# Kernel optimization log

Measured on AMD Instinct MI355X. Metric: run time of the kernel, lower is better.

Reference implementation:

```python
import jax, jax.numpy as jnp
import numpy as np

KS = 5
STRIDE = 1


def extract_patches(x, ks, s):
    # TF tf.image.extract_patches ordering: (row, col, channel) flattened
    B, H, W, C = x.shape
    oh = (H - ks) // s + 1
    ow = (W - ks) // s + 1
    cols = [x[:, i:i + (oh - 1) * s + 1:s, j:j + (ow - 1) * s + 1:s, :]
            for i in range(ks) for j in range(ks)]
    p = jnp.stack(cols, axis=3)  # [B, oh, ow, ks*ks, C]
    return p.reshape(B, oh * ow, ks * ks * C)


def setup_inputs() -> dict:
    key = jax.random.key(0)
    k1, k2, k3 = jax.random.split(key, 3)
    B, H, W, C, K = 32, 14, 14, 32, 64
    mu_in = jax.random.normal(k1, (B, H, W, C), dtype=jnp.float32)
    Sigma_in = jax.random.uniform(k2, (B, H * W, H * W, C), dtype=jnp.float32)
    w_mu = 0.05 * jax.random.normal(k3, (KS, KS, C, K), dtype=jnp.float32)
    w_sigma = jnp.full((K,), -2.2, dtype=jnp.float32)
    return {"mu_in": mu_in, "Sigma_in": Sigma_in, "w_mu": w_mu, "w_sigma": w_sigma}


def reference(mu_in, Sigma_in, w_mu, w_sigma):
    B, H, W, C = mu_in.shape
    ks = w_mu.shape[0]
    K = w_mu.shape[-1]
    s = STRIDE

    # mean path: standard conv2d, NHWC / HWIO
    mu_out = jax.lax.conv_general_dilated(
        mu_in, w_mu, (s, s), 'VALID',
        dimension_numbers=('NHWC', 'HWIO', 'NHWC'))

    # diag of Sigma_in over the two N dims: [B,N,N,C] -> [B,C,N] -> [B,H,W,C]
    diag_sigma = jnp.diagonal(Sigma_in, axis1=1, axis2=2)           # [B,C,N]
    diag_sigma = jnp.transpose(diag_sigma, (0, 2, 1)).reshape(B, H, W, C)

    dsg = extract_patches(diag_sigma, ks, s)                        # [B,P,M]
    P = dsg.shape[1]

    mu_cov_sq = (w_mu * w_mu).reshape(-1, K)                        # [M,K]
    v1 = dsg @ mu_cov_sq                                            # [B,P,K]

    sp = jnp.log1p(jnp.exp(w_sigma))                                # softplus, [K]
    tr = jnp.sum(dsg, axis=2, keepdims=True)                        # [B,P,1]
    diag_vals = v1 + sp[None, None, :] * tr                         # [B,P,K] (trace1 + mu_wT_sigmags_mu_w diags)

    mu_p = extract_patches(mu_in, ks, s)                            # [B,P,M]
    G = jnp.einsum('bpm,bqm->bpq', mu_p, mu_p)                      # [B,P,P]

    Sigma_out = sp[None, None, None, :] * G[..., None]              # [B,P,P,K]
    ip = jnp.arange(P)
    Sigma_out = Sigma_out.at[:, ip, ip, :].add(diag_vals)

    Sigma_out = jnp.where(jnp.isnan(Sigma_out), 0.0, Sigma_out)
    Sigma_out = jnp.where(jnp.isinf(Sigma_out), 0.0, Sigma_out)

    # TF set_diag acts on the LAST two dims ([P,K] inner matrices) -- reproduce exactly
    m = min(P, K)
    ii = jnp.arange(m)
    Sigma_out = Sigma_out.at[:, :, ii, ii].set(jnp.abs(Sigma_out[:, :, ii, ii]))
    return mu_out, Sigma_out
```

## Files before the change

### kernel.cpp

```cpp
#include <hip/hip_runtime.h>
#include <cmath>

typedef __attribute__((ext_vector_type(8))) short short8;
typedef __attribute__((ext_vector_type(4))) float f32x4;

#define NB 32
#define MU_OUT_SZ (NB*100*64)
#define LDAP 56

__device__ inline unsigned short f2bf(float f) {
  unsigned u = __builtin_bit_cast(unsigned, f);
  u += 0x7fffu + ((u >> 16) & 1u);
  return (unsigned short)(u >> 16);
}

__global__ __launch_bounds__(256) void prepW(
    const float* __restrict__ w_mu, const float* __restrict__ w_sigma,
    unsigned short* __restrict__ wf) {
  __shared__ float wsh[2048];
  const int ij = blockIdx.x, t = threadIdx.x;
  const float4* src = (const float4*)(w_mu + (size_t)ij * 2048);
  ((float4*)wsh)[t]       = src[t];
  ((float4*)wsh)[t + 256] = src[t + 256];
  __syncthreads();
#pragma unroll
  for (int id0 = 0; id0 < 512; id0 += 256) {
    const int id = id0 + t;
    const int kind = id >> 8;
    const int rest = id & 255;
    const int n = rest >> 6, l = rest & 63;
    const int col = n * 16 + (l & 15);
    const int m0 = (l >> 4) * 8;
    const float sp = log1pf(expf(w_sigma[col]));
    unsigned short v[8];
#pragma unroll
    for (int i = 0; i < 8; ++i) {
      const float wv = wsh[(m0 + i) * 64 + col];
      const float x = kind ? (wv * wv + sp) : wv;
      v[i] = f2bf(x);
    }
    uint4 pk;
    pk.x = v[0] | ((unsigned)v[1] << 16);
    pk.y = v[2] | ((unsigned)v[3] << 16);
    pk.z = v[4] | ((unsigned)v[5] << 16);
    pk.w = v[6] | ((unsigned)v[7] << 16);
    *(uint4*)(wf + (size_t)((ij * 8 + kind * 4 + n) * 64 + l) * 8) = pk;
  }
}

__global__ __launch_bounds__(512) void fusedK(
    const float* __restrict__ mu_in, const float* __restrict__ Sigma_in,
    const unsigned short* __restrict__ wf, const float* __restrict__ w_sigma,
    float* __restrict__ out) {
  __shared__ unsigned short mu_sh[196 * LDAP];
  __shared__ unsigned short sd_sh[196 * LDAP];
  __shared__ float g_sh[16][100];
  __shared__ float dv_sh[16][64];
  const int r = blockIdx.x;
  const int b = blockIdx.y;
  const int t = threadIdx.x, l = t & 63, w = t >> 6;

  const float4* mu4 = (const float4*)(mu_in + (size_t)b * 6272);
  for (int f = t; f < 1568; f += 512) {
    const float4 v = mu4[f];
    const int row = f >> 3, c = (f & 7) * 4;
    ushort4 pv;
    pv.x = f2bf(v.x); pv.y = f2bf(v.y); pv.z = f2bf(v.z); pv.w = f2bf(v.w);
    *(ushort4*)(mu_sh + row * LDAP + c) = pv;
    const float4 s = *(const float4*)(Sigma_in +
        ((size_t)(b * 196 + row) * 196 + row) * 32 + c);
    ushort4 ps;
    ps.x = f2bf(s.x); ps.y = f2bf(s.y); ps.z = f2bf(s.z); ps.w = f2bf(s.w);
    *(ushort4*)(sd_sh + row * LDAP + c) = ps;
  }
  __syncthreads();

  const int laneP = l & 15, g16 = (l >> 4) * 8;
  const int pA = (r * 16 + laneP > 99) ? 99 : r * 16 + laneP;
  const int baseA = ((pA / 10) * 14 + (pA % 10)) * LDAP + g16;
  const bool doG = (w < 7);
  const int q = w * 16 + laneP;
  const int qc = q > 99 ? 99 : q;
  const int baseB = ((qc / 10) * 14 + (qc % 10)) * LDAP + g16;
  const bool doMu = (w < 4);
  const int n = doMu ? w : (w - 4);
  const int kslot = doMu ? n : (4 + n);

  const short8* wfp = (const short8*)wf;
  short8 fw = wfp[(size_t)kslot * 64 + l];
  f32x4 aG = {}, aX = {};
  for (int ij = 0; ij < 25; ++ij) {
    const short8 fw_n = (ij < 24) ? wfp[(size_t)((ij + 1) * 8 + kslot) * 64 + l] : fw;
    const int off = ((ij / 5) * 14 + (ij % 5)) * LDAP;
    if (doG) {
      const short8 fA = *(const short8*)(mu_sh + baseA + off);
      const short8 fB = *(const short8*)(mu_sh + baseB + off);
      aG = __builtin_amdgcn_mfma_f32_16x16x32_bf16(fA, fB, aG, 0, 0, 0);
      if (doMu) {
        aX = __builtin_amdgcn_mfma_f32_16x16x32_bf16(fA, fw, aX, 0, 0, 0);
      } else {
        const short8 fS = *(const short8*)(sd_sh + baseA + off);
        aX = __builtin_amdgcn_mfma_f32_16x16x32_bf16(fS, fw, aX, 0, 0, 0);
      }
    } else {
      const short8 fS = *(const short8*)(sd_sh + baseA + off);
      aX = __builtin_amdgcn_mfma_f32_16x16x32_bf16(fS, fw, aX, 0, 0, 0);
    }
    fw = fw_n;
  }

  const int prow0 = (l >> 4) * 4;
  if (doG && q < 100) {
#pragma unroll
    for (int j = 0; j < 4; ++j) g_sh[prow0 + j][q] = aG[j];
  }
  const int k = n * 16 + laneP;
  if (doMu) {
    float* mo = out + (size_t)b * 6400;
#pragma unroll
    for (int j = 0; j < 4; ++j) {
      const int p = r * 16 + prow0 + j;
      if (p < 100) mo[p * 64 + k] = aX[j];
    }
  } else {
#pragma unroll
    for (int j = 0; j < 4; ++j) dv_sh[prow0 + j][k] = aX[j];
  }
  __syncthreads();

  const int nrows = (r == 6) ? 4 : 16;
  const int p0 = r * 16;
  const int k4 = (t & 15) * 4;
  const float4 wsv = *(const float4*)(w_sigma + k4);
  f32x4 sp4;
  sp4.x = log1pf(expf(wsv.x));
  sp4.y = log1pf(expf(wsv.y));
  sp4.z = log1pf(expf(wsv.z));
  sp4.w = log1pf(expf(wsv.w));
  float* sig = out + MU_OUT_SZ + ((size_t)(b * 100 + p0) * 100) * 64;
  const int total = nrows * 1600;
  for (int l4 = t; l4 < total; l4 += 512) {
    const int row = l4 / 1600;
    const int rem = l4 - row * 1600;
    const int qq = rem >> 4;
    const float g = g_sh[row][qq];
    f32x4 v;
    v.x = sp4.x * g; v.y = sp4.y * g; v.z = sp4.z * g; v.w = sp4.w * g;
    if (qq == p0 + row) {
      const float4 dvv = *(const float4*)&dv_sh[row][k4];
      v.x += dvv.x; v.y += dvv.y; v.z += dvv.z; v.w += dvv.w;
    }
    v.x = (qq == k4)     ? fabsf(v.x) : v.x;
    v.y = (qq == k4 + 1) ? fabsf(v.y) : v.y;
    v.z = (qq == k4 + 2) ? fabsf(v.z) : v.z;
    v.w = (qq == k4 + 3) ? fabsf(v.w) : v.w;
    __builtin_nontemporal_store(v, (f32x4*)(sig + (size_t)l4 * 4));
  }
}

extern "C" void kernel_launch(void* const* d_in, const int* in_sizes, int n_in,
                              void* d_out, int out_size, void* d_ws, size_t ws_size,
                              hipStream_t stream) {
  const float* mu_in    = (const float*)d_in[0];
  const float* Sigma_in = (const float*)d_in[1];
  const float* w_mu     = (const float*)d_in[2];
  const float* w_sigma  = (const float*)d_in[3];
  float* out = (float*)d_out;
  unsigned short* wf = (unsigned short*)d_ws;

  prepW<<<25, 256, 0, stream>>>(w_mu, w_sigma, wf);
  fusedK<<<dim3(7, NB), 512, 0, stream>>>(mu_in, Sigma_in, wf, w_sigma, out);
}
```

Measured before the change: 33.13 us.

## Split fused kernel across q-halves to double block count

Adds a grid dimension that splits each (row-tile, batch) block into two halves over the q columns of the Gram/Sigma_out output, so 448 blocks run instead of 224. The work of the mean conv and the diagonal-variance MFMA is divided between the halves by row tile, and only the half that needs the Sigma diagonal loads it. The aim is better occupancy of the CUs for a kernel dominated by large output stores. The cost is duplicated mu staging per half and more complex per-wave role logic.

After: 33.83 us. 2.1% more time.

```diff
diff --git a/kernel.cpp b/kernel.cpp
--- a/kernel.cpp
+++ b/kernel.cpp
@@ -48,17 +48,20 @@
   }
 }
 
-__global__ __launch_bounds__(512) void fusedK(
+__global__ __launch_bounds__(512) void fusedH(
     const float* __restrict__ mu_in, const float* __restrict__ Sigma_in,
     const unsigned short* __restrict__ wf, const float* __restrict__ w_sigma,
     float* __restrict__ out) {
   __shared__ unsigned short mu_sh[196 * LDAP];
   __shared__ unsigned short sd_sh[196 * LDAP];
-  __shared__ float g_sh[16][100];
+  __shared__ float g_sh[16][64];
   __shared__ float dv_sh[16][64];
   const int r = blockIdx.x;
-  const int b = blockIdx.y;
+  const int zh = blockIdx.y;
+  const int b = blockIdx.z;
   const int t = threadIdx.x, l = t & 63, w = t >> 6;
+  const int p0 = r * 16;
+  const bool hasDv = (zh == 0) ? (r <= 3) : (r >= 4);
 
   const float4* mu4 = (const float4*)(mu_in + (size_t)b * 6272);
   for (int f = t; f < 1568; f += 512) {
@@ -67,69 +70,81 @@
     ushort4 pv;
     pv.x = f2bf(v.x); pv.y = f2bf(v.y); pv.z = f2bf(v.z); pv.w = f2bf(v.w);
     *(ushort4*)(mu_sh + row * LDAP + c) = pv;
-    const float4 s = *(const float4*)(Sigma_in +
-        ((size_t)(b * 196 + row) * 196 + row) * 32 + c);
-    ushort4 ps;
-    ps.x = f2bf(s.x); ps.y = f2bf(s.y); ps.z = f2bf(s.z); ps.w = f2bf(s.w);
-    *(ushort4*)(sd_sh + row * LDAP + c) = ps;
+  }
+  if (hasDv) {
+    for (int f = t; f < 1568; f += 512) {
+      const int row = f >> 3, c = (f & 7) * 4;
+      const float4 s = *(const float4*)(Sigma_in +
+          ((size_t)(b * 196 + row) * 196 + row) * 32 + c);
+      ushort4 ps;
+      ps.x = f2bf(s.x); ps.y = f2bf(s.y); ps.z = f2bf(s.z); ps.w = f2bf(s.w);
+      *(ushort4*)(sd_sh + row * LDAP + c) = ps;
+    }
   }
   __syncthreads();
 
   const int laneP = l & 15, g16 = (l >> 4) * 8;
-  const int pA = (r * 16 + laneP > 99) ? 99 : r * 16 + laneP;
+  const int pA = (p0 + laneP > 99) ? 99 : p0 + laneP;
   const int baseA = ((pA / 10) * 14 + (pA % 10)) * LDAP + g16;
-  const bool doG = (w < 7);
-  const int q = w * 16 + laneP;
-  const int qc = q > 99 ? 99 : q;
-  const int baseB = ((qc / 10) * 14 + (qc % 10)) * LDAP + g16;
-  const bool doMu = (w < 4);
-  const int n = doMu ? w : (w - 4);
-  const int kslot = doMu ? n : (4 + n);
+  const int gT = (zh == 0) ? ((w < 4) ? w : -1) : ((w < 3) ? 4 + w : -1);
+  const int sn = (zh == 0) ? ((w >= 4) ? w - 4 : -1)
+                           : ((w >= 3 && w < 7) ? w - 3 : -1);
+  int qg = 0, baseB = 0;
+  if (gT >= 0) {
+    qg = gT * 16 + laneP;
+    const int qc = qg > 99 ? 99 : qg;
+    baseB = ((qc / 10) * 14 + (qc % 10)) * LDAP + g16;
+  }
+  const int kslot = (sn >= 0) ? (hasDv ? 4 + sn : sn) : 0;
 
   const short8* wfp = (const short8*)wf;
-  short8 fw = wfp[(size_t)kslot * 64 + l];
+  short8 fw = {};
+  if (sn >= 0) fw = wfp[(size_t)kslot * 64 + l];
   f32x4 aG = {}, aX = {};
   for (int ij = 0; ij < 25; ++ij) {
-    const short8 fw_n = (ij < 24) ? wfp[(size_t)((ij + 1) * 8 + kslot) * 64 + l] : fw;
+    short8 fw_n = fw;
+    if (sn >= 0 && ij < 24) fw_n = wfp[(size_t)((ij + 1) * 8 + kslot) * 64 + l];
     const int off = ((ij / 5) * 14 + (ij % 5)) * LDAP;
-    if (doG) {
+    if (gT >= 0) {
       const short8 fA = *(const short8*)(mu_sh + baseA + off);
       const short8 fB = *(const short8*)(mu_sh + baseB + off);
       aG = __builtin_amdgcn_mfma_f32_16x16x32_bf16(fA, fB, aG, 0, 0, 0);
-      if (doMu) {
-        aX = __builtin_amdgcn_mfma_f32_16x16x32_bf16(fA, fw, aX, 0, 0, 0);
-      } else {
+    }
+    if (sn >= 0) {
+      if (hasDv) {
         const short8 fS = *(const short8*)(sd_sh + baseA + off);
         aX = __builtin_amdgcn_mfma_f32_16x16x32_bf16(fS, fw, aX, 0, 0, 0);
-      }
+      } else {
+        const short8 fA = *(const short8*)(mu_sh + baseA + off);
+        aX = __builtin_amdgcn_mfma_f32_16x16x32_bf16(fA, fw, aX, 0, 0, 0);
+      }
+    }
+    fw = fw_n;
+  }
+
+  const int prow0 = (l >> 4) * 4;
+  if (gT >= 0 && qg < 100) {
+    const int ql = qg - zh * 64;
+#pragma unroll
+    for (int j = 0; j < 4; ++j) g_sh[prow0 + j][ql] = aG[j];
+  }
+  if (sn >= 0) {
+    const int k = sn * 16 + laneP;
+    if (hasDv) {
+#pragma unroll
+      for (int j = 0; j < 4; ++j) dv_sh[prow0 + j][k] = aX[j];
     } else {
-      const short8 fS = *(const short8*)(sd_sh + baseA + off);
-      aX = __builtin_amdgcn_mfma_f32_16x16x32_bf16(fS, fw, aX, 0, 0, 0);
-    }
-    fw = fw_n;
-  }
-
-  const int prow0 = (l >> 4) * 4;
-  if (doG && q < 100) {
-#pragma unroll
-    for (int j = 0; j < 4; ++j) g_sh[prow0 + j][q] = aG[j];
-  }
-  const int k = n * 16 + laneP;
-  if (doMu) {
-    float* mo = out + (size_t)b * 6400;
-#pragma unroll
-    for (int j = 0; j < 4; ++j) {
-      const int p = r * 16 + prow0 + j;
-      if (p < 100) mo[p * 64 + k] = aX[j];
-    }
-  } else {
-#pragma unroll
-    for (int j = 0; j < 4; ++j) dv_sh[prow0 + j][k] = aX[j];
+      float* mo = out + (size_t)b * 6400;
+#pragma unroll
+      for (int j = 0; j < 4; ++j) {
+        const int p = p0 + prow0 + j;
+        if (p < 100) mo[p * 64 + k] = aX[j];
+      }
+    }
   }
   __syncthreads();
 
   const int nrows = (r == 6) ? 4 : 16;
-  const int p0 = r * 16;
   const int k4 = (t & 15) * 4;
   const float4 wsv = *(const float4*)(w_sigma + k4);
   f32x4 sp4;
@@ -137,24 +152,45 @@
   sp4.y = log1pf(expf(wsv.y));
   sp4.z = log1pf(expf(wsv.z));
   sp4.w = log1pf(expf(wsv.w));
-  float* sig = out + MU_OUT_SZ + ((size_t)(b * 100 + p0) * 100) * 64;
-  const int total = nrows * 1600;
-  for (int l4 = t; l4 < total; l4 += 512) {
-    const int row = l4 / 1600;
-    const int rem = l4 - row * 1600;
-    const int qq = rem >> 4;
-    const float g = g_sh[row][qq];
-    f32x4 v;
-    v.x = sp4.x * g; v.y = sp4.y * g; v.z = sp4.z * g; v.w = sp4.w * g;
-    if (qq == p0 + row) {
-      const float4 dvv = *(const float4*)&dv_sh[row][k4];
-      v.x += dvv.x; v.y += dvv.y; v.z += dvv.z; v.w += dvv.w;
-    }
-    v.x = (qq == k4)     ? fabsf(v.x) : v.x;
-    v.y = (qq == k4 + 1) ? fabsf(v.y) : v.y;
-    v.z = (qq == k4 + 2) ? fabsf(v.z) : v.z;
-    v.w = (qq == k4 + 3) ? fabsf(v.w) : v.w;
-    __builtin_nontemporal_store(v, (f32x4*)(sig + (size_t)l4 * 4));
+  float* sig0 = out + MU_OUT_SZ + (size_t)(b * 100 + p0) * 6400 + zh * 64 * 64;
+
+  if (zh == 0) {
+    for (int row = 0; row < nrows; ++row) {
+      const bool dvRow = hasDv && (p0 + row < 64);
+      float* rowp = sig0 + (size_t)row * 6400;
+#pragma unroll
+      for (int s = 0; s < 2; ++s) {
+        const int idx = t + s * 512;
+        const int ql = idx >> 4;
+        const float g = g_sh[row][ql];
+        f32x4 v;
+        v.x = sp4.x * g; v.y = sp4.y * g; v.z = sp4.z * g; v.w = sp4.w * g;
+        if (dvRow && ql == p0 + row) {
+          const float4 dvv = *(const float4*)&dv_sh[row][k4];
+          v.x += dvv.x; v.y += dvv.y; v.z += dvv.z; v.w += dvv.w;
+        }
+        v.x = (ql == k4)     ? fabsf(v.x) : v.x;
+        v.y = (ql == k4 + 1) ? fabsf(v.y) : v.y;
+        v.z = (ql == k4 + 2) ? fabsf(v.z) : v.z;
+        v.w = (ql == k4 + 3) ? fabsf(v.w) : v.w;
+        __builtin_nontemporal_store(v, (f32x4*)(rowp + (size_t)idx * 4));
+      }
+    }
+  } else {
+    for (int row = 0; row < nrows; ++row) {
+      float* rowp = sig0 + (size_t)row * 6400;
+      for (int idx = t; idx < 576; idx += 512) {
+        const int ql = idx >> 4;
+        const float g = g_sh[row][ql];
+        f32x4 v;
+        v.x = sp4.x * g; v.y = sp4.y * g; v.z = sp4.z * g; v.w = sp4.w * g;
+        if (hasDv && 64 + ql == p0 + row) {
+          const float4 dvv = *(const float4*)&dv_sh[row][k4];
+          v.x += dvv.x; v.y += dvv.y; v.z += dvv.z; v.w += dvv.w;
+        }
+        __builtin_nontemporal_store(v, (f32x4*)(rowp + (size_t)idx * 4));
+      }
+    }
   }
 }
 
@@ -169,5 +205,5 @@
   unsigned short* wf = (unsigned short*)d_ws;
 
   prepW<<<25, 256, 0, stream>>>(w_mu, w_sigma, wf);
-  fusedK<<<dim3(7, NB), 512, 0, stream>>>(mu_in, Sigma_in, wf, w_sigma, out);
-}
+  fusedH<<<dim3(7, 2, NB), 512, 0, stream>>>(mu_in, Sigma_in, wf, w_sigma, out);
+}
```
